# Kernel optimization log

Measured on AMD Instinct MI355X. Metric: run time of the kernel, lower is better.

The kernel has to match this reference:

```python
import jax, jax.numpy as jnp
import numpy as np

IN_F, OUT_F = 4096, 4096
GROUP = 128
N_GROUPS = IN_F // GROUP
R, NUM_A, NUM_B = 16, 2, 2
LORA_ALPHA = 32
SCALING = LORA_ALPHA / R  # 2.0
BITS = 4
PACK = 32 // BITS  # 8 int4 per int32


def dequant_gptq(qweight, qzeros, scales, g_idx):
    """Unpack int4 GPTQ weights -> dense [in_features, out_features] fp32."""
    shifts = (jnp.arange(PACK, dtype=jnp.int32) * BITS)
    # qweight: [in/8, out] packed along in dim
    wq = (qweight[:, None, :] >> shifts[None, :, None]) & 0xF       # [in/8, 8, out]
    wq = wq.reshape(IN_F, OUT_F).astype(jnp.float32)
    # qzeros: [n_groups, out/8] packed along out dim
    zq = (qzeros[:, :, None] >> shifts[None, None, :]) & 0xF        # [g, out/8, 8]
    zq = zq.reshape(N_GROUPS, OUT_F).astype(jnp.float32)
    # per-row group lookup
    return scales[g_idx] * (wq - zq[g_idx])                          # [in, out]


def activation_weights(x, normalize=True):
    # 'inps' mode: per-input-feature importance from mean |activation|
    w = jnp.mean(jnp.abs(x), axis=tuple(range(x.ndim - 1)))          # [in]
    if normalize:
        w = w / (jnp.mean(w) + 1e-6)
    return w


def setup_inputs() -> dict:
    key = jax.random.key(0)
    ks = jax.random.split(key, 8)
    x = jax.random.normal(ks[0], (2, 2048, IN_F), dtype=jnp.float32)
    scales = jax.random.uniform(ks[1], (N_GROUPS, OUT_F), dtype=jnp.float32) * 0.01 + 0.001
    bias = jax.random.normal(ks[2], (OUT_F,), dtype=jnp.float32) * 0.01
    lora_A = jax.random.normal(ks[3], (NUM_A, R, IN_F), dtype=jnp.float32) * (1.0 / np.sqrt(IN_F))
    lora_B = jax.random.normal(ks[4], (NUM_B, OUT_F, R), dtype=jnp.float32) * 0.01
    qweight = jax.random.randint(ks[5], (IN_F // PACK, OUT_F), 0, 2147483647, dtype=jnp.int32)
    qzeros = jax.random.randint(ks[6], (N_GROUPS, OUT_F // PACK), 0, 2147483647, dtype=jnp.int32)
    g_idx = (jnp.arange(IN_F, dtype=jnp.int32) // GROUP).astype(jnp.int32)
    return {"x": x, "scales": scales, "bias": bias, "lora_A": lora_A,
            "lora_B": lora_B, "qweight": qweight, "qzeros": qzeros, "g_idx": g_idx}


def reference(x, scales, bias, lora_A, lora_B, qweight, qzeros, g_idx):
    W = dequant_gptq(qweight, qzeros, scales, g_idx)                 # [in, out]
    result = jnp.einsum('bsi,io->bso', x, W) + bias                  # base GPTQ linear
    # activation-aware 'inps' weighting (dropout p=0 -> identity, eval mode)
    aw = activation_weights(x, normalize=True)                       # [in]
    x_w = x * aw                                                     # broadcast on last dim
    # sum_{i,j} B_j(A_i(x_w)) == (sum_j B_j) @ (sum_i A_i) @ x_w (all linear, no bias)
    A_sum = jnp.sum(lora_A, axis=0)                                  # [r, in]
    B_sum = jnp.sum(lora_B, axis=0)                                  # [out, r]
    h = jnp.einsum('bsi,ri->bsr', x_w, A_sum)                        # [b, s, r]
    result = result + jnp.einsum('bsr,or->bso', h, B_sum) * SCALING
    return result
```

## Files before the change

kernel.cpp:

```cpp
#include <hip/hip_runtime.h>
#include <stdint.h>

#define IN_F 4096
#define OUT_F 4096

typedef __attribute__((ext_vector_type(4))) float f32x4;
typedef _Float16 f16x8 __attribute__((ext_vector_type(8)));
typedef _Float16 f16x2 __attribute__((ext_vector_type(2)));
typedef unsigned short u16x8 __attribute__((ext_vector_type(8)));

__device__ __forceinline__ unsigned short f2h(float f) {
  _Float16 h = (_Float16)f;
  return __builtin_bit_cast(unsigned short, h);
}

#define SIGMA_TAB 0x73625140u

#define OFF_XH     ((size_t)0)
#define OFF_PART   ((size_t)33554432)
#define OFF_W      ((size_t)35651584)
#define OFF_BSUM   ((size_t)35667968)
#define OFF_AW     ((size_t)35668480)
#define OFF_BS     ((size_t)35799552)
#define OFF_HPART  ((size_t)36061696)
#define OFF_HB     ((size_t)38158848)
#define WS_NEED    ((size_t)38420992)

__global__ __launch_bounds__(256) void k1_prep(const float* __restrict__ x,
                                               unsigned short* __restrict__ xh,
                                               float* __restrict__ part) {
  int t = threadIdx.x;
  int c8 = (blockIdx.x * 256 + t) * 8;
  int by = blockIdx.y;
  float a[8];
  #pragma unroll
  for (int i = 0; i < 8; ++i) a[i] = 0.f;
  for (int rr = 0; rr < 32; ++rr) {
    size_t off = (size_t)(by * 32 + rr) * IN_F + c8;
    f32x4 v0 = *(const f32x4*)(x + off);
    f32x4 v1 = *(const f32x4*)(x + off + 4);
    u16x8 o;
    o[0] = f2h(v0[0]); o[1] = f2h(v1[0]); o[2] = f2h(v0[1]); o[3] = f2h(v1[1]);
    o[4] = f2h(v0[2]); o[5] = f2h(v1[2]); o[6] = f2h(v0[3]); o[7] = f2h(v1[3]);
    *(u16x8*)(xh + off) = o;
    a[0] += fabsf(v0[0]); a[1] += fabsf(v0[1]); a[2] += fabsf(v0[2]); a[3] += fabsf(v0[3]);
    a[4] += fabsf(v1[0]); a[5] += fabsf(v1[1]); a[6] += fabsf(v1[2]); a[7] += fabsf(v1[3]);
  }
  f32x4 p0 = { a[0], a[1], a[2], a[3] };
  f32x4 p1 = { a[4], a[5], a[6], a[7] };
  *(f32x4*)(part + (size_t)by * IN_F + c8) = p0;
  *(f32x4*)(part + (size_t)by * IN_F + c8 + 4) = p1;
}

__global__ __launch_bounds__(256) void k2_colred(const float* __restrict__ part,
                                                 float* __restrict__ w,
                                                 float* __restrict__ bsum) {
  int t = threadIdx.x;
  int col = blockIdx.x * 256 + t;
  float s = 0.f;
  for (int st = 0; st < 128; ++st) s += part[(size_t)st * IN_F + col];
  float wv = s * (1.0f / 4096.0f);
  w[col] = wv;
  __shared__ float red[256];
  red[t] = wv; __syncthreads();
  for (int k = 128; k > 0; k >>= 1) { if (t < k) red[t] += red[t + k]; __syncthreads(); }
  if (t == 0) bsum[blockIdx.x] = red[0];
}

__global__ __launch_bounds__(256) void k3_fold(const float* __restrict__ lora_A,
                                               const float* __restrict__ lora_B,
                                               const float* __restrict__ w,
                                               const float* __restrict__ bsum,
                                               unsigned short* __restrict__ A_w,
                                               unsigned short* __restrict__ Bs) {
  int b = blockIdx.x, t = threadIdx.x;
  float s = 0.f;
  #pragma unroll
  for (int i = 0; i < 16; ++i) s += bsum[i];
  float iv = 1.0f / (s * (1.0f / 4096.0f) + 1e-6f);
  if (b < 256) {
    int idx = b * 256 + t;
    int r = idx >> 12;
    int pos = idx & 4095;
    int p = pos & 7;
    int orig = (pos & ~7) + (int)((SIGMA_TAB >> (p * 4)) & 7);
    float v = (lora_A[(size_t)r * IN_F + orig] + lora_A[(size_t)(16 + r) * IN_F + orig]) * w[orig] * iv;
    A_w[idx] = f2h(v);
  } else {
    int idx = (b - 256) * 256 + t;
    int o = idx >> 5, r = idx & 31;
    float v = 0.f;
    if (r < 16) v = 2.0f * (lora_B[o * 16 + r] + lora_B[OUT_F * 16 + o * 16 + r]);
    Bs[idx] = f2h(v);
  }
}

__global__ __launch_bounds__(256) void k4_h(const unsigned short* __restrict__ xh,
                                            const unsigned short* __restrict__ A_w,
                                            float* __restrict__ hpart) {
  int mb = blockIdx.x, kc = blockIdx.y;
  int t = threadIdx.x, wid = t >> 6, l = t & 63;
  int m0 = mb * 128 + wid * 32;
  int lr = l & 15, lg = l >> 4;
  f32x4 z = { 0.f, 0.f, 0.f, 0.f };
  f32x4 acc0 = z, acc1 = z;
  for (int it = 0; it < 16; ++it) {
    int k = kc * 512 + it * 32 + lg * 8;
    f16x8 b  = *(const f16x8*)(A_w + (size_t)lr * IN_F + k);
    f16x8 a0 = *(const f16x8*)(xh + (size_t)(m0 + lr) * IN_F + k);
    f16x8 a1 = *(const f16x8*)(xh + (size_t)(m0 + 16 + lr) * IN_F + k);
    acc0 = __builtin_amdgcn_mfma_f32_16x16x32_f16(a0, b, acc0, 0, 0, 0);
    acc1 = __builtin_amdgcn_mfma_f32_16x16x32_f16(a1, b, acc1, 0, 0, 0);
  }
  float* hp = hpart + (size_t)kc * IN_F * 16;
  #pragma unroll
  for (int r = 0; r < 4; ++r) {
    hp[(size_t)(m0 + lg * 4 + r) * 16 + lr]      = acc0[r];
    hp[(size_t)(m0 + 16 + lg * 4 + r) * 16 + lr] = acc1[r];
  }
}

__global__ __launch_bounds__(256) void k5_hred(const float* __restrict__ hpart,
                                               unsigned short* __restrict__ hb) {
  int gid = blockIdx.x * 256 + threadIdx.x;
  int m = gid >> 5, r = gid & 31;
  float v = 0.f;
  if (r < 16)
    for (int kc = 0; kc < 8; ++kc) v += hpart[(size_t)kc * 65536 + m * 16 + r];
  hb[gid] = f2h(v);
}

__device__ __forceinline__ f16x8 deq8(unsigned int q, f16x2 s2, f16x2 zz2) {
  unsigned int u0 = ( q         & 0x000F000Fu) | 0x64006400u;
  unsigned int u1 = ((q >> 4)   & 0x000F000Fu) | 0x64006400u;
  unsigned int u2 = ((q >> 8)   & 0x000F000Fu) | 0x64006400u;
  unsigned int u3 = ((q >> 12)  & 0x000F000Fu) | 0x64006400u;
  f16x2 w0 = (__builtin_bit_cast(f16x2, u0) - zz2) * s2;
  f16x2 w1 = (__builtin_bit_cast(f16x2, u1) - zz2) * s2;
  f16x2 w2 = (__builtin_bit_cast(f16x2, u2) - zz2) * s2;
  f16x2 w3 = (__builtin_bit_cast(f16x2, u3) - zz2) * s2;
  struct { f16x2 a, b, c, d; } r { w0, w1, w2, w3 };
  return __builtin_bit_cast(f16x8, r);
}

__global__ __launch_bounds__(256) void k6_gemm(const unsigned short* __restrict__ xh,
                                               const int* __restrict__ qweight,
                                               const int* __restrict__ qzeros,
                                               const float* __restrict__ scales,
                                               const float* __restrict__ bias,
                                               const unsigned short* __restrict__ hb,
                                               const unsigned short* __restrict__ Bs,
                                               float* __restrict__ out) {
  __shared__ __align__(16) unsigned short As[2][128 * 128];
  int t = threadIdx.x, wid = t >> 6, l = t & 63;
  int lr = l & 15, lg = l >> 4;
  int b0 = blockIdx.x;
  int bid = (b0 & 7) * 128 + (b0 >> 3);
  int mt = bid >> 5, nt = bid & 31;
  int m0 = mt * 128, n0 = nt * 128;
  int wm = wid >> 1, wn = wid & 1;
  int mrow0 = wm * 64;
  int ncol0 = n0 + wn * 64 + lr;

  f32x4 zz = { 0.f, 0.f, 0.f, 0.f };
  f32x4 acc[4][4];
  #pragma unroll
  for (int m = 0; m < 4; ++m)
    #pragma unroll
    for (int j = 0; j < 4; ++j) acc[m][j] = zz;

  int row0 = t >> 4;
  int cp = (t & 15) ^ row0;
  const unsigned short* aE = xh + (size_t)(m0 + row0) * IN_F + cp * 8;
  const int*   qE = qweight + (size_t)lg * OUT_F + ncol0;
  const float* sE = scales + ncol0;
  const int*   zE = qzeros + (ncol0 >> 3);
  int zsh = (lr & 7) * 4;

  #define STAGE_A(BUF, APTR) do {                                                 \
    _Pragma("unroll")                                                             \
    for (int it = 0; it < 8; ++it) {                                              \
      const unsigned short* gp = (APTR) + (size_t)it * 16 * IN_F;                 \
      __builtin_amdgcn_global_load_lds((const __attribute__((address_space(1))) void*)gp, \
                                       (__attribute__((address_space(3))) void*)(&As[BUF][0] + (it * 256 + t) * 8), \
                                       16, 0, 0);                                 \
    }                                                                             \
  } while (0)

  #define LOAD_QW(QW, QPTR) do {                                                  \
    _Pragma("unroll")                                                             \
    for (int ks = 0; ks < 4; ++ks)                                                \
      _Pragma("unroll")                                                           \
      for (int j = 0; j < 4; ++j)                                                 \
        QW[j][ks] = (unsigned int)(QPTR)[ks * 4 * OUT_F + j * 16];                \
  } while (0)

  #define LOAD_CONST(S2, ZP, SPTR, ZPTR) do {                                     \
    _Pragma("unroll")                                                             \
    for (int j = 0; j < 4; ++j) {                                                 \
      float s_ = (SPTR)[j * 16];                                                  \
      unsigned int zi = (unsigned int)(ZPTR)[j * 2];                              \
      unsigned int z = (zi >> zsh) & 0xFu;                                        \
      unsigned int zzu = 0x64006400u + z * 0x00010001u;                           \
      ZP[j] = __builtin_bit_cast(f16x2, zzu);                                     \
      _Float16 sh = (_Float16)s_;                                                 \
      unsigned int sb = (unsigned int)__builtin_bit_cast(unsigned short, sh);     \
      unsigned int ssu = (sb << 16) | sb;                                         \
      S2[j] = __builtin_bit_cast(f16x2, ssu);                                     \
    }                                                                             \
  } while (0)

  #define COMPUTE(BUF, QW, S2, ZP) do {                                           \
    _Pragma("unroll")                                                             \
    for (int ks = 0; ks < 4; ++ks) {                                              \
      f16x8 bf[4];                                                                \
      _Pragma("unroll")                                                           \
      for (int j = 0; j < 4; ++j)                                                 \
        bf[j] = deq8(QW[j][ks], S2[j], ZP[j]);                                    \
      f16x8 a[4];                                                                 \
      int chunk = (ks * 4 + lg) ^ lr;                                             \
      _Pragma("unroll")                                                           \
      for (int m = 0; m < 4; ++m)                                                 \
        a[m] = *(const f16x8*)(&As[BUF][0] + (mrow0 + m * 16 + lr) * 128 + chunk * 8); \
      __builtin_amdgcn_s_setprio(1);                                              \
      _Pragma("unroll")                                                           \
      for (int m = 0; m < 4; ++m)                                                 \
        _Pragma("unroll")                                                         \
        for (int j = 0; j < 4; ++j)                                               \
          acc[m][j] = __builtin_amdgcn_mfma_f32_16x16x32_f16(a[m], bf[j], acc[m][j], 0, 0, 0); \
      __builtin_amdgcn_s_setprio(0);                                              \
    }                                                                             \
  } while (0)

  unsigned int qwA[4][4], qwB[4][4];
  f16x2 s2a[4], zpa[4], s2b[4], zpb[4];

  STAGE_A(0, aE);
  LOAD_QW(qwA, qE);
  LOAD_CONST(s2a, zpa, sE, zE);
  const unsigned short* aO = aE + 128;
  const int*   qO = qE + 16 * OUT_F;
  const float* sO = sE + OUT_F;
  const int*   zO = zE + OUT_F / 8;
  aE += 256; qE += 32 * OUT_F; sE += 2 * OUT_F; zE += 2 * (OUT_F / 8);
  __syncthreads();

  for (int kt = 0; kt < 32; kt += 2) {
    LOAD_QW(qwB, qO);
    LOAD_CONST(s2b, zpb, sO, zO);
    STAGE_A(1, aO);
    COMPUTE(0, qwA, s2a, zpa);
    __syncthreads();
    if (kt + 2 < 32) {
      LOAD_QW(qwA, qE);
      LOAD_CONST(s2a, zpa, sE, zE);
      STAGE_A(0, aE);
    }
    COMPUTE(1, qwB, s2b, zpb);
    __syncthreads();
    aO += 256; qO += 32 * OUT_F; sO += 2 * OUT_F; zO += 2 * (OUT_F / 8);
    aE += 256; qE += 32 * OUT_F; sE += 2 * OUT_F; zE += 2 * (OUT_F / 8);
  }
  #undef STAGE_A
  #undef LOAD_QW
  #undef LOAD_CONST
  #undef COMPUTE

  {
    f16x8 bb[4];
    #pragma unroll
    for (int j = 0; j < 4; ++j)
      bb[j] = *(const f16x8*)(Bs + (size_t)(ncol0 + j * 16) * 32 + lg * 8);
    #pragma unroll
    for (int m = 0; m < 4; ++m) {
      f16x8 ah = *(const f16x8*)(hb + (size_t)(m0 + mrow0 + m * 16 + lr) * 32 + lg * 8);
      #pragma unroll
      for (int j = 0; j < 4; ++j)
        acc[m][j] = __builtin_amdgcn_mfma_f32_16x16x32_f16(ah, bb[j], acc[m][j], 0, 0, 0);
    }
  }
  #pragma unroll
  for (int j = 0; j < 4; ++j) {
    int ocol = ncol0 + j * 16;
    float bv = bias[ocol];
    #pragma unroll
    for (int m = 0; m < 4; ++m) {
      int orow = m0 + mrow0 + m * 16 + lg * 4;
      #pragma unroll
      for (int r = 0; r < 4; ++r)
        out[(size_t)(orow + r) * OUT_F + ocol] = acc[m][j][r] + bv;
    }
  }
}

extern "C" void kernel_launch(void* const* d_in, const int* in_sizes, int n_in,
                              void* d_out, int out_size, void* d_ws, size_t ws_size,
                              hipStream_t stream) {
  const float* x       = (const float*)d_in[0];
  const float* scales  = (const float*)d_in[1];
  const float* bias    = (const float*)d_in[2];
  const float* lora_A  = (const float*)d_in[3];
  const float* lora_B  = (const float*)d_in[4];
  const int*   qweight = (const int*)d_in[5];
  const int*   qzeros  = (const int*)d_in[6];
  float* out = (float*)d_out;

  if (ws_size < WS_NEED) return;

  char* ws = (char*)d_ws;
  unsigned short* xh  = (unsigned short*)(ws + OFF_XH);
  float* part         = (float*)(ws + OFF_PART);
  float* w            = (float*)(ws + OFF_W);
  float* bsum         = (float*)(ws + OFF_BSUM);
  unsigned short* A_w = (unsigned short*)(ws + OFF_AW);
  unsigned short* Bs  = (unsigned short*)(ws + OFF_BS);
  float* hpart        = (float*)(ws + OFF_HPART);
  unsigned short* hb  = (unsigned short*)(ws + OFF_HB);

  k1_prep<<<dim3(2, 128), 256, 0, stream>>>(x, xh, part);
  k2_colred<<<16, 256, 0, stream>>>(part, w, bsum);
  k3_fold<<<768, 256, 0, stream>>>(lora_A, lora_B, w, bsum, A_w, Bs);
  k4_h<<<dim3(32, 8), 256, 0, stream>>>(xh, A_w, hpart);
  k5_hred<<<512, 256, 0, stream>>>(hpart, hb);
  k6_gemm<<<1024, 256, 0, stream>>>(xh, qweight, qzeros, scales, bias, hb, Bs, out);
}
```

Before: 202.5 us.

## Switch GEMM to 32x32x16 MFMA with per-wave column strips

Replaces the 16x16x32 MFMA tiling, where each wave owned a 64x64 subtile, with 32x32x16 MFMA where each wave owns the full 128 rows by a 32-column strip. Each lane now dequantizes one column (8 packed words per k-tile instead of 16), which cuts redundant dequant work and scale/zero loads per wave. In exchange, every wave reads all 128 rows of A from LDS, so LDS traffic rises. The output store pattern also changes to match the 32x32 accumulator layout.

```diff
diff --git a/kernel.cpp b/kernel.cpp
--- a/kernel.cpp
+++ b/kernel.cpp
@@ -5,6 +5,7 @@
 #define OUT_F 4096
 
 typedef __attribute__((ext_vector_type(4))) float f32x4;
+typedef __attribute__((ext_vector_type(16))) float f32x16;
 typedef _Float16 f16x8 __attribute__((ext_vector_type(8)));
 typedef _Float16 f16x2 __attribute__((ext_vector_type(2)));
 typedef unsigned short u16x8 __attribute__((ext_vector_type(8)));
@@ -152,30 +153,29 @@
                                                const unsigned short* __restrict__ Bs,
                                                float* __restrict__ out) {
   __shared__ __align__(16) unsigned short As[2][128 * 128];
-  int t = threadIdx.x, wid = t >> 6, l = t & 63;
-  int lr = l & 15, lg = l >> 4;
+  int t = threadIdx.x, w = t >> 6, l = t & 63;
+  int lr = l & 15;
+  int lc = l & 31;
+  int hi = l >> 5;
   int b0 = blockIdx.x;
   int bid = (b0 & 7) * 128 + (b0 >> 3);
   int mt = bid >> 5, nt = bid & 31;
   int m0 = mt * 128, n0 = nt * 128;
-  int wm = wid >> 1, wn = wid & 1;
-  int mrow0 = wm * 64;
-  int ncol0 = n0 + wn * 64 + lr;
-
-  f32x4 zz = { 0.f, 0.f, 0.f, 0.f };
-  f32x4 acc[4][4];
+  int ncol = n0 + w * 32 + lc;
+
+  f32x16 acc[4];
   #pragma unroll
   for (int m = 0; m < 4; ++m)
     #pragma unroll
-    for (int j = 0; j < 4; ++j) acc[m][j] = zz;
+    for (int r = 0; r < 16; ++r) acc[m][r] = 0.f;
 
   int row0 = t >> 4;
   int cp = (t & 15) ^ row0;
   const unsigned short* aE = xh + (size_t)(m0 + row0) * IN_F + cp * 8;
-  const int*   qE = qweight + (size_t)lg * OUT_F + ncol0;
-  const float* sE = scales + ncol0;
-  const int*   zE = qzeros + (ncol0 >> 3);
-  int zsh = (lr & 7) * 4;
+  const int*   qE = qweight + (size_t)hi * OUT_F + ncol;
+  const float* sE = scales + ncol;
+  const int*   zE = qzeros + (ncol >> 3);
+  int zsh = (l & 7) * 4;
 
   #define STAGE_A(BUF, APTR) do {                                                 \
     _Pragma("unroll")                                                             \
@@ -189,51 +189,41 @@
 
   #define LOAD_QW(QW, QPTR) do {                                                  \
     _Pragma("unroll")                                                             \
-    for (int ks = 0; ks < 4; ++ks)                                                \
-      _Pragma("unroll")                                                           \
-      for (int j = 0; j < 4; ++j)                                                 \
-        QW[j][ks] = (unsigned int)(QPTR)[ks * 4 * OUT_F + j * 16];                \
+    for (int ks = 0; ks < 8; ++ks)                                                \
+      QW[ks] = (unsigned int)(QPTR)[ks * 2 * OUT_F];                              \
   } while (0)
 
   #define LOAD_CONST(S2, ZP, SPTR, ZPTR) do {                                     \
-    _Pragma("unroll")                                                             \
-    for (int j = 0; j < 4; ++j) {                                                 \
-      float s_ = (SPTR)[j * 16];                                                  \
-      unsigned int zi = (unsigned int)(ZPTR)[j * 2];                              \
-      unsigned int z = (zi >> zsh) & 0xFu;                                        \
-      unsigned int zzu = 0x64006400u + z * 0x00010001u;                           \
-      ZP[j] = __builtin_bit_cast(f16x2, zzu);                                     \
-      _Float16 sh = (_Float16)s_;                                                 \
-      unsigned int sb = (unsigned int)__builtin_bit_cast(unsigned short, sh);     \
-      unsigned int ssu = (sb << 16) | sb;                                         \
-      S2[j] = __builtin_bit_cast(f16x2, ssu);                                     \
-    }                                                                             \
+    float s_ = (SPTR)[0];                                                         \
+    unsigned int zi = (unsigned int)(ZPTR)[0];                                    \
+    unsigned int z = (zi >> zsh) & 0xFu;                                          \
+    unsigned int zzu = 0x64006400u + z * 0x00010001u;                             \
+    ZP = __builtin_bit_cast(f16x2, zzu);                                          \
+    _Float16 sh = (_Float16)s_;                                                   \
+    unsigned int sb = (unsigned int)__builtin_bit_cast(unsigned short, sh);       \
+    unsigned int ssu = (sb << 16) | sb;                                           \
+    S2 = __builtin_bit_cast(f16x2, ssu);                                          \
   } while (0)
 
   #define COMPUTE(BUF, QW, S2, ZP) do {                                           \
     _Pragma("unroll")                                                             \
-    for (int ks = 0; ks < 4; ++ks) {                                              \
-      f16x8 bf[4];                                                                \
-      _Pragma("unroll")                                                           \
-      for (int j = 0; j < 4; ++j)                                                 \
-        bf[j] = deq8(QW[j][ks], S2[j], ZP[j]);                                    \
+    for (int ks = 0; ks < 8; ++ks) {                                              \
+      f16x8 bf = deq8(QW[ks], S2, ZP);                                            \
+      int chunk_ = (ks * 2 + hi) ^ lr;                                            \
       f16x8 a[4];                                                                 \
-      int chunk = (ks * 4 + lg) ^ lr;                                             \
       _Pragma("unroll")                                                           \
       for (int m = 0; m < 4; ++m)                                                 \
-        a[m] = *(const f16x8*)(&As[BUF][0] + (mrow0 + m * 16 + lr) * 128 + chunk * 8); \
+        a[m] = *(const f16x8*)(&As[BUF][0] + (m * 32 + lc) * 128 + chunk_ * 8);   \
       __builtin_amdgcn_s_setprio(1);                                              \
       _Pragma("unroll")                                                           \
       for (int m = 0; m < 4; ++m)                                                 \
-        _Pragma("unroll")                                                         \
-        for (int j = 0; j < 4; ++j)                                               \
-          acc[m][j] = __builtin_amdgcn_mfma_f32_16x16x32_f16(a[m], bf[j], acc[m][j], 0, 0, 0); \
+        acc[m] = __builtin_amdgcn_mfma_f32_32x32x16_f16(a[m], bf, acc[m], 0, 0, 0); \
       __builtin_amdgcn_s_setprio(0);                                              \
     }                                                                             \
   } while (0)
 
-  unsigned int qwA[4][4], qwB[4][4];
-  f16x2 s2a[4], zpa[4], s2b[4], zpb[4];
+  unsigned int qwA[8], qwB[8];
+  f16x2 s2a, zpa, s2b, zpb;
 
   STAGE_A(0, aE);
   LOAD_QW(qwA, qE);
@@ -267,28 +257,23 @@
   #undef COMPUTE
 
   {
-    f16x8 bb[4];
-    #pragma unroll
-    for (int j = 0; j < 4; ++j)
-      bb[j] = *(const f16x8*)(Bs + (size_t)(ncol0 + j * 16) * 32 + lg * 8);
+    f16x8 bb = *(const f16x8*)(Bs + (size_t)ncol * 32 + hi * 8);
     #pragma unroll
     for (int m = 0; m < 4; ++m) {
-      f16x8 ah = *(const f16x8*)(hb + (size_t)(m0 + mrow0 + m * 16 + lr) * 32 + lg * 8);
-      #pragma unroll
-      for (int j = 0; j < 4; ++j)
-        acc[m][j] = __builtin_amdgcn_mfma_f32_16x16x32_f16(ah, bb[j], acc[m][j], 0, 0, 0);
+      f16x8 ah = *(const f16x8*)(hb + (size_t)(m0 + m * 32 + lc) * 32 + hi * 8);
+      acc[m] = __builtin_amdgcn_mfma_f32_32x32x16_f16(ah, bb, acc[m], 0, 0, 0);
     }
   }
-  #pragma unroll
-  for (int j = 0; j < 4; ++j) {
-    int ocol = ncol0 + j * 16;
-    float bv = bias[ocol];
+  {
+    float bv = bias[ncol];
     #pragma unroll
     for (int m = 0; m < 4; ++m) {
-      int orow = m0 + mrow0 + m * 16 + lg * 4;
+      int rbase = m0 + m * 32 + 4 * hi;
       #pragma unroll
-      for (int r = 0; r < 4; ++r)
-        out[(size_t)(orow + r) * OUT_F + ocol] = acc[m][j][r] + bv;
+      for (int r = 0; r < 16; ++r) {
+        int orow = rbase + (r & 3) + 8 * (r >> 2);
+        out[(size_t)orow * OUT_F + ncol] = acc[m][r] + bv;
+      }
     }
   }
 }
```

Result: faster. 187.9 us (-7.2%).
